# Kernel tuning notes

Hardware: AMD Instinct MI355X
Metric: run time of the kernel (lower is better)

## Reference

```python
import jax, jax.numpy as jnp
import numpy as np

N_QUBITS = 10
DEPTH = 5
DIM = 2 ** N_QUBITS  # 1024
NUM_CLASSES = 2
BATCH = 16384
IN_DIM = 784


def _rot_matrices(w):
    # w: [depth, n_qubits, 3] angles (phi, theta, omega); qml.Rot = RZ(omega) RY(theta) RZ(phi)
    phi, theta, omega = w[..., 0], w[..., 1], w[..., 2]
    c, s = jnp.cos(theta / 2), jnp.sin(theta / 2)
    e = lambda a: jnp.exp(1j * a.astype(jnp.complex64))
    m00 = e(-(phi + omega) / 2) * c
    m01 = -e((phi - omega) / 2) * s
    m10 = e(-(phi - omega) / 2) * s
    m11 = e((phi + omega) / 2) * c
    return jnp.stack([jnp.stack([m00, m01], -1), jnp.stack([m10, m11], -1)], -2)  # [D, n, 2, 2]


def _apply_1q(state, U, w):
    # state: [B] + [2]*n ; apply 2x2 U on qubit axis w
    s = jnp.moveaxis(state, w + 1, -1)
    s = s @ U.T
    return jnp.moveaxis(s, -1, w + 1)


def _apply_cnot(state, c, t):
    s = jnp.moveaxis(state, (c + 1, t + 1), (-2, -1))
    s = jnp.concatenate([s[..., 0:1, :], s[..., 1:2, ::-1]], axis=-2)  # flip target where control=1
    return jnp.moveaxis(s, (-2, -1), (c + 1, t + 1))


def _circuit(x, weights):
    B = x.shape[0]
    # AmplitudeEmbedding: pad_with=0, normalize=True
    amp = jnp.pad(x, ((0, 0), (0, DIM - x.shape[1])))
    amp = amp / jnp.linalg.norm(amp, axis=1, keepdims=True)
    state = amp.astype(jnp.complex64).reshape((B,) + (2,) * N_QUBITS)
    U = _rot_matrices(weights)
    for d in range(DEPTH):
        for i in range(N_QUBITS):  # entangling CNOT ring
            state = _apply_cnot(state, i, (i + 1) % N_QUBITS)
        for i in range(N_QUBITS):  # per-qubit Rot
            state = _apply_1q(state, U[d, i], i)
    probs = (state.real ** 2 + state.imag ** 2).reshape(B, DIM)
    # <Z_i> = P(bit_i = 0) - P(bit_i = 1)
    z = []
    for i in range(N_QUBITS):
        p = probs.reshape(B, 2 ** i, 2, -1)
        z.append(p[:, :, 0, :].sum((1, 2)) - p[:, :, 1, :].sum((1, 2)))
    return jnp.stack(z, axis=1)  # [B, n_qubits]


def setup_inputs() -> dict:
    key = jax.random.key(0)
    k1, k2, k3 = jax.random.split(key, 3)
    x = jax.random.normal(k1, (BATCH, IN_DIM), dtype=jnp.float32)
    weights = jax.random.uniform(k2, (DEPTH, N_QUBITS, 3), dtype=jnp.float32) * (2.0 * np.pi)
    y = jax.random.randint(k3, (BATCH,), 0, NUM_CLASSES)
    return {"x": x, "weights": weights, "y": y}


def reference(x, weights, y):
    logits = _circuit(x, weights)[:, :NUM_CLASSES]
    logp = jax.nn.log_softmax(logits, axis=-1)
    loss = -jnp.take_along_axis(logp, y[:, None], axis=1).mean()
    return loss
```

## Files before the change

### kernel.cpp

```cpp
#include <hip/hip_runtime.h>
#include <type_traits>

#define NQ 10
#define N_DEPTH 5
#define DIM 1024
#define BATCH 16384
#define IN_DIM 784
#define NGATES 50
#define KALLOC 832
#define NT 13
#define NSLOT 768
#define NB 12

typedef float f32x2 __attribute__((ext_vector_type(2)));
typedef float f32x4 __attribute__((ext_vector_type(4)));
typedef unsigned u32x4 __attribute__((ext_vector_type(4)));

struct MaskTab {
  unsigned v[NGATES];
  unsigned p[NGATES];
  unsigned vz0, vz1;
};

constexpr MaskTab make_masks() {
  MaskTab t{};
  unsigned v[NQ], p[NQ];
  for (int i = 0; i < NQ; ++i) { v[i] = 1u << (9 - i); p[i] = 1u << (9 - i); }
  for (int d = 0; d < N_DEPTH; ++d) {
    for (int i = 0; i < NQ; ++i) {
      int c = i, tt = (i + 1) % NQ;
      v[tt] ^= v[c];
      p[c]  ^= p[tt];
    }
    for (int i = 0; i < NQ; ++i) {
      t.v[d * NQ + i] = v[i];
      t.p[d * NQ + i] = p[i];
    }
  }
  t.vz0 = v[0];
  t.vz1 = v[1];
  return t;
}

constexpr MaskTab MT = make_masks();

struct PermTab { short slot[DIM]; };
constexpr PermTab make_perm() {
  PermTab t{};
  int a = 0, b = 256, c = 512;
  for (int m = 0; m < DIM; ++m) {
    const int p0 = __builtin_popcount((unsigned)m & MT.vz0) & 1;
    const int p1 = __builtin_popcount((unsigned)m & MT.vz1) & 1;
    if (p0 && !p1)      t.slot[m] = (short)a++;
    else if (!p0 && p1) t.slot[m] = (short)b++;
    else if (p0 && p1)  t.slot[m] = (short)c++;
    else                t.slot[m] = -1;
  }
  return t;
}
__constant__ PermTab d_PT = make_perm();

struct BitPlan { int wpos[2]; int rpos[2]; int lpos[6]; unsigned wmask; };
constexpr BitPlan make_plan() {
  BitPlan bp{};
  int bestc = 1000; unsigned best = 3;
  for (int a = 0; a < NQ; ++a)
    for (int b = a + 1; b < NQ; ++b) {
      unsigned m = (1u << a) | (1u << b);
      int c = 0;
      for (int g = 0; g < NGATES; ++g) if (MT.p[g] & m) ++c;
      if (c < bestc) { bestc = c; best = m; }
    }
  bp.wmask = best;
  int rem[NQ]; int nr = 0, wi = 0;
  for (int b = 0; b < NQ; ++b) {
    if (best & (1u << b)) bp.wpos[wi++] = b;
    else rem[nr++] = b;
  }
  for (int i = 0; i < 6; ++i) bp.lpos[i] = rem[i];
  bp.rpos[0] = rem[6]; bp.rpos[1] = rem[7];
  return bp;
}
constexpr BitPlan BP = make_plan();

constexpr unsigned gath_l(unsigned p) {
  unsigned r = 0;
  for (int i = 0; i < 6; ++i) if (p & (1u << BP.lpos[i])) r |= 1u << i;
  return r;
}
constexpr unsigned gath_r(unsigned p) {
  unsigned r = 0;
  for (int i = 0; i < 2; ++i) if (p & (1u << BP.rpos[i])) r |= 1u << i;
  return r;
}
constexpr unsigned scat_r(unsigned x) {
  return ((x & 1u) << BP.rpos[0]) | (((x >> 1) & 1u) << BP.rpos[1]);
}
constexpr int ncross_before(int g) {
  int c = 0;
  for (int i = 0; i < g; ++i) if (MT.p[i] & BP.wmask) ++c;
  return c;
}

template <int I, int N, typename F>
__device__ __forceinline__ void static_for(F&& f) {
  if constexpr (I < N) {
    f(std::integral_constant<int, I>{});
    static_for<I + 1, N>(static_cast<F&&>(f));
  }
}

constexpr int xcost(unsigned m) {
  constexpr int t[16] = {0,1,1,1,2,2,2,1,1,2,2,2,2,2,2,1};
  return t[m & 15u] + (((m >> 4) & 1u) ? 3 : 0) + (((m >> 5) & 1u) ? 3 : 0);
}

template <int CTRL>
__device__ __forceinline__ float dppf(float x) {
  int xi = (int)__float_as_uint(x);
  return __uint_as_float(
      (unsigned)__builtin_amdgcn_update_dpp(xi, xi, CTRL, 0xF, 0xF, false));
}

__device__ __forceinline__ float plswap16(float x) {
  float a = x, b = x;
  asm("s_nop 1\n\t"
      "v_permlane16_swap_b32 %0, %1" : "+v"(a), "+v"(b));
  return (a + b) - x;
}
__device__ __forceinline__ float plswap32(float x) {
  float a = x, b = x;
  asm("s_nop 1\n\t"
      "v_permlane32_swap_b32 %0, %1" : "+v"(a), "+v"(b));
  return (a + b) - x;
}

template <unsigned M>
__device__ __forceinline__ float xlane_f(float x) {
  float r = x;
  constexpr unsigned m4 = M & 15u;
  if constexpr (m4 == 1u)  r = dppf<0x0B1>(r);
  else if constexpr (m4 == 2u)  r = dppf<0x04E>(r);
  else if constexpr (m4 == 3u)  r = dppf<0x01B>(r);
  else if constexpr (m4 == 4u)  { r = dppf<0x141>(r); r = dppf<0x01B>(r); }
  else if constexpr (m4 == 5u)  { r = dppf<0x141>(r); r = dppf<0x04E>(r); }
  else if constexpr (m4 == 6u)  { r = dppf<0x141>(r); r = dppf<0x0B1>(r); }
  else if constexpr (m4 == 7u)  r = dppf<0x141>(r);
  else if constexpr (m4 == 8u)  r = dppf<0x128>(r);
  else if constexpr (m4 == 9u)  { r = dppf<0x128>(r); r = dppf<0x0B1>(r); }
  else if constexpr (m4 == 10u) { r = dppf<0x128>(r); r = dppf<0x04E>(r); }
  else if constexpr (m4 == 11u) { r = dppf<0x128>(r); r = dppf<0x01B>(r); }
  else if constexpr (m4 == 12u) { r = dppf<0x140>(r); r = dppf<0x01B>(r); }
  else if constexpr (m4 == 13u) { r = dppf<0x140>(r); r = dppf<0x04E>(r); }
  else if constexpr (m4 == 14u) { r = dppf<0x140>(r); r = dppf<0x0B1>(r); }
  else if constexpr (m4 == 15u) r = dppf<0x140>(r);
  if constexpr ((M & 16u) != 0u) r = plswap16(r);
  if constexpr ((M & 32u) != 0u) r = plswap32(r);
  return r;
}

template <unsigned M>
__device__ __forceinline__ f32x2 xchg(f32x2 v) {
  if constexpr (M == 0u) {
    return v;
  } else if constexpr (xcost(M) >= 5) {
    f32x2 r;
    r.x = __shfl_xor(v.x, (int)M);
    r.y = __shfl_xor(v.y, (int)M);
    return r;
  } else {
    f32x2 r;
    r.x = xlane_f<M>(v.x);
    r.y = xlane_f<M>(v.y);
    return r;
  }
}

__device__ __forceinline__ f32x2 ampfma(f32x2 o, f32x2 q, f32x2 co, f32x2 cp) {
  f32x2 d;
  asm("v_pk_mul_f32 %0, %2, %1 op_sel:[0,0] op_sel_hi:[0,1]\n\t"
      "v_pk_fma_f32 %0, %2, %1, %0 op_sel:[1,1,0] op_sel_hi:[1,0,1] neg_lo:[1,0,0]\n\t"
      "v_pk_fma_f32 %0, %3, %4, %0 op_sel:[0,0,0] op_sel_hi:[0,1,1]\n\t"
      "v_pk_fma_f32 %0, %3, %4, %0 op_sel:[1,1,0] op_sel_hi:[1,0,1] neg_lo:[1,0,0]"
      : "=&v"(d)
      : "v"(o), "v"(co), "v"(cp), "v"(q));
  return d;
}

__device__ __forceinline__ float fxor(float x, unsigned m) {
  return __uint_as_float(__float_as_uint(x) ^ m);
}

__device__ __forceinline__ unsigned pk4_fp8(float a, float b, float c, float d) {
  int v = __builtin_amdgcn_cvt_pk_fp8_f32(a, b, 0, false);
  v = __builtin_amdgcn_cvt_pk_fp8_f32(c, d, v, true);
  return (unsigned)v;
}

__device__ __forceinline__ void gll16(const void* g, void* l) {
  __builtin_amdgcn_global_load_lds(
      (const __attribute__((address_space(1))) void*)g,
      (__attribute__((address_space(3))) void*)l, 16, 0, 0);
}

#define XSCALE 32.0f
#define WSCALE 16.0f
#define SINV   (1.0f / 262144.0f)

__global__ __launch_bounds__(256) void prep(const float* __restrict__ X,
                                            char* __restrict__ Xf8,
                                            float* __restrict__ xn2,
                                            const float* __restrict__ w,
                                            unsigned short* __restrict__ W2u) {
  __shared__ f32x4 UL4[NGATES];
  __shared__ f32x2 S0[DIM];
  __shared__ f32x2 S1[DIM];

  const int tid = threadIdx.x;

  if (blockIdx.x >= 832) {
    const int row = (blockIdx.x - 832) * 8 + (tid >> 5);
    const int l32 = tid & 31;
    const float* src = X + (size_t)row * IN_DIM;
    char* dst = Xf8 + (size_t)row * KALLOC;
    float ssq = 0.0f;
    for (int c = l32; c < 52; c += 32) {
      u32x4 out;
      if (c < 49) {
        f32x4 v0 = *(const f32x4*)(src + c * 16);
        f32x4 v1 = *(const f32x4*)(src + c * 16 + 4);
        f32x4 v2 = *(const f32x4*)(src + c * 16 + 8);
        f32x4 v3 = *(const f32x4*)(src + c * 16 + 12);
        ssq += v0.x * v0.x + v0.y * v0.y + v0.z * v0.z + v0.w * v0.w +
               v1.x * v1.x + v1.y * v1.y + v1.z * v1.z + v1.w * v1.w +
               v2.x * v2.x + v2.y * v2.y + v2.z * v2.z + v2.w * v2.w +
               v3.x * v3.x + v3.y * v3.y + v3.z * v3.z + v3.w * v3.w;
        out = u32x4{
          pk4_fp8(v0.x * XSCALE, v0.y * XSCALE, v0.z * XSCALE, v0.w * XSCALE),
          pk4_fp8(v1.x * XSCALE, v1.y * XSCALE, v1.z * XSCALE, v1.w * XSCALE),
          pk4_fp8(v2.x * XSCALE, v2.y * XSCALE, v2.z * XSCALE, v2.w * XSCALE),
          pk4_fp8(v3.x * XSCALE, v3.y * XSCALE, v3.z * XSCALE, v3.w * XSCALE)};
      } else {
        out = u32x4{0, 0, 0, 0};
      }
      *(u32x4*)(dst + c * 16) = out;
    }
#pragma unroll
    for (int off = 1; off < 32; off <<= 1) ssq += __shfl_xor(ssq, off);
    if (l32 == 0) xn2[row] = ssq;
    return;
  }

  if (tid < NGATES) {
    float phi = w[tid * 3 + 0], th = w[tid * 3 + 1], om = w[tid * 3 + 2];
    float ct = cosf(th * 0.5f), st = sinf(th * 0.5f);
    float aa = (phi + om) * 0.5f, bb = (phi - om) * 0.5f;
    float cA = cosf(aa), sA = sinf(aa), cB = cosf(bb), sB = sinf(bb);
    UL4[tid] = f32x4{ ct * cA, -ct * sA, -st * cB, -st * sB };
  }

  const int j = blockIdx.x;
  unsigned short* rowp = W2u + (size_t)j * NSLOT;

  if (j >= IN_DIM) {
#pragma unroll
    for (int k = 0; k < 3; ++k) rowp[tid + k * 256] = 0;
    return;
  }

  const int wv = tid >> 6, lane = tid & 63;
  unsigned mbase = ((unsigned)(wv & 1) << BP.wpos[0]) |
                   ((unsigned)(wv >> 1) << BP.wpos[1]);
#pragma unroll
  for (int i = 0; i < 6; ++i)
    mbase |= (((unsigned)lane >> i) & 1u) << BP.lpos[i];

  f32x2 a[4];
  static_for<0, 4>([&](auto R_) {
    constexpr int r = decltype(R_)::value;
    constexpr unsigned rs = scat_r((unsigned)r);
    a[r] = f32x2{((mbase | rs) == (unsigned)j) ? 1.0f : 0.0f, 0.0f};
  });
  __syncthreads();

  static_for<0, NGATES>([&](auto G_) {
    constexpr int G = decltype(G_)::value;
    constexpr unsigned p = MT.p[G];
    constexpr unsigned v = MT.v[G];
    constexpr unsigned pw = p & BP.wmask;
    const f32x4 A = UL4[G];

    if constexpr (pw == 0u) {
      constexpr unsigned lx = gath_l(p);
      constexpr unsigned rx = gath_r(p);
      if constexpr (rx == 0u) {
        static_for<0, 4>([&](auto R_) {
          constexpr int r = decltype(R_)::value;
          constexpr unsigned rs = scat_r((unsigned)r);
          f32x2 o = a[r];
          f32x2 q = xchg<lx>(o);
          const unsigned sg =
              (unsigned)(__popc((int)((mbase | rs) & v)) & 1) << 31;
          const f32x2 co = {A.x, fxor(A.y, sg)};
          const f32x2 cp = {fxor(A.z, sg), A.w};
          a[r] = ampfma(o, q, co, cp);
        });
      } else {
        static_for<0, 4>([&](auto R_) {
          constexpr int r = decltype(R_)::value;
          constexpr int r2 = r ^ (int)rx;
          if constexpr (r < r2) {
            constexpr unsigned rs0 = scat_r((unsigned)r);
            constexpr unsigned rs1 = scat_r((unsigned)r2);
            f32x2 o0 = a[r], o1 = a[r2];
            f32x2 q0 = xchg<lx>(o1);
            f32x2 q1 = xchg<lx>(o0);
            const unsigned sg0 =
                (unsigned)(__popc((int)((mbase | rs0) & v)) & 1) << 31;
            const unsigned sg1 =
                (unsigned)(__popc((int)((mbase | rs1) & v)) & 1) << 31;
            const f32x2 co0 = {A.x, fxor(A.y, sg0)};
            const f32x2 cp0 = {fxor(A.z, sg0), A.w};
            const f32x2 co1 = {A.x, fxor(A.y, sg1)};
            const f32x2 cp1 = {fxor(A.z, sg1), A.w};
            a[r]  = ampfma(o0, q0, co0, cp0);
            a[r2] = ampfma(o1, q1, co1, cp1);
          }
        });
      }
    } else {
      constexpr int cidx = ncross_before(G);
      f32x2* S = (cidx & 1) ? S1 : S0;
      static_for<0, 4>([&](auto R_) {
        constexpr int r = decltype(R_)::value;
        constexpr unsigned rs = scat_r((unsigned)r);
        S[mbase | rs] = a[r];
      });
      __syncthreads();
      static_for<0, 4>([&](auto R_) {
        constexpr int r = decltype(R_)::value;
        constexpr unsigned rs = scat_r((unsigned)r);
        const unsigned m = mbase | rs;
        f32x2 o = a[r];
        f32x2 q = S[m ^ p];
        const unsigned sg = (unsigned)(__popc((int)(m & v)) & 1) << 31;
        const f32x2 co = {A.x, fxor(A.y, sg)};
        const f32x2 cp = {fxor(A.z, sg), A.w};
        a[r] = ampfma(o, q, co, cp);
      });
    }
  });

  static_for<0, 4>([&](auto R_) {
    constexpr int r = decltype(R_)::value;
    constexpr unsigned rs = scat_r((unsigned)r);
    const unsigned m = mbase | rs;
    const int s = d_PT.slot[m];
    if (s >= 0)
      rowp[s] = (unsigned short)(pk4_fp8(a[r].x * WSCALE, a[r].y * WSCALE,
                                         0.0f, 0.0f) & 0xffffu);
  });
}

__global__ __launch_bounds__(256) void transpose_w(const unsigned* __restrict__ W2u32,
                                                   unsigned* __restrict__ W2Tu32) {
  __shared__ unsigned tile[64][33];
  const int j0 = blockIdx.x * 64;
  const int s0 = blockIdx.y * 64;
  const int t = threadIdx.x;
#pragma unroll
  for (int i = 0; i < 8; ++i) {
    const int idx = i * 256 + t;
    const int jr = idx >> 5, sc = idx & 31;
    tile[jr][sc] = W2u32[(size_t)(j0 + jr) * (NSLOT / 2) + (s0 >> 1) + sc];
  }
  __syncthreads();
#pragma unroll
  for (int i = 0; i < 8; ++i) {
    const int idx = i * 256 + t;
    const int rl = idx >> 4, jq = idx & 15;
    const int slot = rl >> 1, c = rl & 1;
    const int sc = slot >> 1, p = slot & 1;
    unsigned out = 0;
#pragma unroll
    for (int q = 0; q < 4; ++q) {
      const unsigned w32 = tile[jq * 4 + q][sc];
      const unsigned h = (w32 >> (16 * p)) & 0xffffu;
      out |= ((h >> (8 * c)) & 0xffu) << (8 * q);
    }
    const int orow = 2 * (s0 + slot) + c;
    W2Tu32[((size_t)orow * KALLOC + j0 + jq * 4) >> 2] = out;
  }
}

__global__ __launch_bounds__(512) void gemm_fused(const char* __restrict__ Xf8,
                                                  const char* __restrict__ W2T,
                                                  float* __restrict__ accb) {
  __shared__ u32x4 lds4[3072];
  char* lds = (char*)lds4;

  const int tid = threadIdx.x;
  const int orig = blockIdx.x;
  const int bx = (orig & 7) * 96 + (orig >> 3);
  const int mb = bx / NB, nb = bx % NB;
  const int m0 = mb * 256, n0 = nb * 128;
  const int lane = tid & 63, wv = tid >> 6;
  const int wm = wv >> 2, wn = wv & 3;

  const int rl = lane >> 2;
  const int csrc = (lane & 3) ^ (rl & 3) ^ ((rl >> 2) & 3);

  auto stage = [&](int t) {
    char* Ab = lds + (t & 1) * 24576;
    char* Bb = Ab + 16384;
    const int col = t * 64 + csrc * 16;
#pragma unroll
    for (int i = 0; i < 2; ++i) {
      const int g = wv * 2 + i;
      const int row = g * 16 + rl;
      gll16(Xf8 + (size_t)(m0 + row) * KALLOC + col, Ab + g * 1024);
    }
    {
      const int row = wv * 16 + rl;
      gll16(W2T + (size_t)(n0 + row) * KALLOC + col, Bb + wv * 1024);
    }
  };

  stage(0);
  asm volatile("s_waitcnt vmcnt(0)" ::: "memory");
  __builtin_amdgcn_s_barrier();

  f32x4 acc[8][2];
#pragma unroll
  for (int fm = 0; fm < 8; ++fm)
#pragma unroll
    for (int fn = 0; fn < 2; ++fn) acc[fm][fn] = f32x4{0, 0, 0, 0};

  const int kc = lane >> 4;

  for (int t = 0; t < NT; ++t) {
    const char* Ab = lds + (t & 1) * 24576;
    const char* Bb = Ab + 16384;

    long af0[8], bf0[2], af1[8], bf1[2];
#pragma unroll
    for (int f = 0; f < 8; ++f) {
      const int ar = wm * 128 + f * 16 + (lane & 15);
      const int sw = (ar & 3) ^ ((ar >> 2) & 3);
      af0[f] = *(const long*)(Ab + ar * 64 + (((kc >> 1) ^ sw) * 16) + (kc & 1) * 8);
    }
#pragma unroll
    for (int f = 0; f < 2; ++f) {
      const int br = wn * 32 + f * 16 + (lane & 15);
      const int sw = (br & 3) ^ ((br >> 2) & 3);
      bf0[f] = *(const long*)(Bb + br * 64 + (((kc >> 1) ^ sw) * 16) + (kc & 1) * 8);
    }
    if (t < NT - 1) stage(t + 1);
#pragma unroll
    for (int f = 0; f < 8; ++f) {
      const int ar = wm * 128 + f * 16 + (lane & 15);
      const int sw = (ar & 3) ^ ((ar >> 2) & 3);
      const int kb = 4 + kc;
      af1[f] = *(const long*)(Ab + ar * 64 + (((kb >> 1) ^ sw) * 16) + (kb & 1) * 8);
    }
#pragma unroll
    for (int f = 0; f < 2; ++f) {
      const int br = wn * 32 + f * 16 + (lane & 15);
      const int sw = (br & 3) ^ ((br >> 2) & 3);
      const int kb = 4 + kc;
      bf1[f] = *(const long*)(Bb + br * 64 + (((kb >> 1) ^ sw) * 16) + (kb & 1) * 8);
    }

    __builtin_amdgcn_s_setprio(1);
#pragma unroll
    for (int fm = 0; fm < 8; ++fm)
#pragma unroll
      for (int fn = 0; fn < 2; ++fn)
        acc[fm][fn] = __builtin_amdgcn_mfma_f32_16x16x32_fp8_fp8(
            af0[fm], bf0[fn], acc[fm][fn], 0, 0, 0);
    __builtin_amdgcn_s_setprio(0);

    __builtin_amdgcn_s_setprio(1);
#pragma unroll
    for (int fm = 0; fm < 8; ++fm)
#pragma unroll
      for (int fn = 0; fn < 2; ++fn)
        acc[fm][fn] = __builtin_amdgcn_mfma_f32_16x16x32_fp8_fp8(
            af1[fm], bf1[fn], acc[fm][fn], 0, 0, 0);
    __builtin_amdgcn_s_setprio(0);

    if (t < NT - 1) {
      asm volatile("s_waitcnt vmcnt(0)" ::: "memory");
      __builtin_amdgcn_sched_barrier(0);
      __builtin_amdgcn_s_barrier();
    }
  }

#pragma unroll
  for (int fm = 0; fm < 8; ++fm) {
    float sn[4] = {0, 0, 0, 0};
#pragma unroll
    for (int fn = 0; fn < 2; ++fn) {
#pragma unroll
      for (int r = 0; r < 4; ++r) {
        const float vv = acc[fm][fn][r];
        sn[r] = fmaf(vv, vv, sn[r]);
      }
    }
#pragma unroll
    for (int off = 1; off < 16; off <<= 1) {
#pragma unroll
      for (int r = 0; r < 4; ++r) sn[r] += __shfl_xor(sn[r], off);
    }
    if ((lane & 15) == 0) {
#pragma unroll
      for (int r = 0; r < 4; ++r) {
        const int m = m0 + wm * 128 + fm * 16 + (lane >> 4) * 4 + r;
        accb[(size_t)nb * BATCH + m] = sn[r];
      }
    }
  }
}

__global__ __launch_bounds__(256) void loss_partial(const float* __restrict__ accb,
                                                    const float* __restrict__ xn2,
                                                    const int* __restrict__ y,
                                                    float* __restrict__ partial) {
  const int s = blockIdx.x * 256 + threadIdx.x;
  float SA = 0.0f, SB = 0.0f, SC = 0.0f;
#pragma unroll
  for (int k = 0; k < 4; ++k) {
    SA += accb[(size_t)(0 + k) * BATCH + s];
    SB += accb[(size_t)(4 + k) * BATCH + s];
    SC += accb[(size_t)(8 + k) * BATCH + s];
  }
  SA *= SINV; SB *= SINV; SC *= SINV;
  const float n2 = xn2[s];
  const float z0 = n2 - 2.0f * (SA + SC);
  const float z1 = n2 - 2.0f * (SB + SC);
  const float inv = 1.0f / n2;
  const float l0 = z0 * inv, l1 = z1 * inv;
  const float mx = fmaxf(l0, l1);
  const float lse = mx + logf(expf(l0 - mx) + expf(l1 - mx));
  float loss = lse - ((y[s] == 0) ? l0 : l1);

  __shared__ float sm[256];
  sm[threadIdx.x] = loss;
  __syncthreads();
  for (int st = 128; st > 0; st >>= 1) {
    if (threadIdx.x < st) sm[threadIdx.x] += sm[threadIdx.x + st];
    __syncthreads();
  }
  if (threadIdx.x == 0) partial[blockIdx.x] = sm[0];
}

__global__ __launch_bounds__(64) void loss_final(const float* __restrict__ partial,
                                                 float* __restrict__ out) {
  float v = partial[threadIdx.x];
#pragma unroll
  for (int off = 1; off < 64; off <<= 1) v += __shfl_xor(v, off);
  if (threadIdx.x == 0) out[0] = v * (1.0f / (float)BATCH);
}

extern "C" void kernel_launch(void* const* d_in, const int* in_sizes, int n_in,
                              void* d_out, int out_size, void* d_ws, size_t ws_size,
                              hipStream_t stream) {
  const float* x = (const float*)d_in[0];
  const float* w = (const float*)d_in[1];
  const int*   y = (const int*)d_in[2];

  char* ws = (char*)d_ws;
  char*     Xf8  = ws;
  unsigned short* W2u = (unsigned short*)(ws + 13631488);
  char*     W2Tu = ws + 14909440;
  float*    xn2  = (float*)(ws + 16187392);
  float*    accb = (float*)(ws + 16252928);
  float* partial = (float*)(ws + 17039360);

  prep<<<2880, 256, 0, stream>>>(x, Xf8, xn2, w, W2u);
  transpose_w<<<dim3(13, 12), 256, 0, stream>>>((const unsigned*)W2u,
                                                (unsigned*)W2Tu);
  gemm_fused<<<768, 512, 0, stream>>>(Xf8, W2Tu, accb);
  loss_partial<<<BATCH / 256, 256, 0, stream>>>(accb, xn2, y, partial);
  loss_final<<<1, 64, 0, stream>>>(partial, (float*)d_out);
}
```

Measured before the change: 77.10 us.

## Switch GEMM to scaled 16x16x128 FP8 MFMA with K padded to 896

The fp8 GEMM now uses the MI355X scaled MFMA 16x16x128 instruction with unit scales in place of pairs of 16x16x32 fp8 MFMAs. K is padded from 832 to 896 so it splits into 7 tiles of 128, and transpose_w gains a block that zero-fills the new padding. The LDS tile layout changes to 128-byte rows with an XOR swizzle. The double-buffered prefetch is replaced by a single buffer with load, wait, barrier, compute on each tile, so global loads no longer overlap MFMA work. This trades fewer, wider MFMA issues for lost load/compute overlap and some extra padded K work.

```diff
diff --git a/kernel.cpp b/kernel.cpp
--- a/kernel.cpp
+++ b/kernel.cpp
@@ -7,14 +7,15 @@
 #define BATCH 16384
 #define IN_DIM 784
 #define NGATES 50
-#define KALLOC 832
-#define NT 13
+#define KALLOC 896
+#define NTK 7
 #define NSLOT 768
 #define NB 12
 
 typedef float f32x2 __attribute__((ext_vector_type(2)));
 typedef float f32x4 __attribute__((ext_vector_type(4)));
 typedef unsigned u32x4 __attribute__((ext_vector_type(4)));
+typedef int i32x8 __attribute__((ext_vector_type(8)));
 
 struct MaskTab {
   unsigned v[NGATES];
@@ -206,6 +207,7 @@
 #define XSCALE 32.0f
 #define WSCALE 16.0f
 #define SINV   (1.0f / 262144.0f)
+#define UNIT_SCALE 0x7F7F7F7F
 
 __global__ __launch_bounds__(256) void prep(const float* __restrict__ X,
                                             char* __restrict__ Xf8,
@@ -224,7 +226,7 @@
     const float* src = X + (size_t)row * IN_DIM;
     char* dst = Xf8 + (size_t)row * KALLOC;
     float ssq = 0.0f;
-    for (int c = l32; c < 52; c += 32) {
+    for (int c = l32; c < 56; c += 32) {
       u32x4 out;
       if (c < 49) {
         f32x4 v0 = *(const f32x4*)(src + c * 16);
@@ -368,6 +370,18 @@
   const int j0 = blockIdx.x * 64;
   const int s0 = blockIdx.y * 64;
   const int t = threadIdx.x;
+
+  if (j0 == 832) {
+#pragma unroll
+    for (int i = 0; i < 8; ++i) {
+      const int idx = i * 256 + t;
+      const int rl = idx >> 4, jq = idx & 15;
+      const int orow = 2 * s0 + rl;
+      W2Tu32[((size_t)orow * KALLOC + 832 + jq * 4) >> 2] = 0u;
+    }
+    return;
+  }
+
 #pragma unroll
   for (int i = 0; i < 8; ++i) {
     const int idx = i * 256 + t;
@@ -407,68 +421,63 @@
   const int lane = tid & 63, wv = tid >> 6;
   const int wm = wv >> 2, wn = wv & 3;
 
-  const int rl = lane >> 2;
-  const int csrc = (lane & 3) ^ (rl & 3) ^ ((rl >> 2) & 3);
+  const int rl = lane >> 3;
+  const int csrc = (lane & 7) ^ rl;
+
+  char* Ab = lds;
+  char* Bb = lds + 32768;
 
   auto stage = [&](int t) {
-    char* Ab = lds + (t & 1) * 24576;
-    char* Bb = Ab + 16384;
-    const int col = t * 64 + csrc * 16;
+    const int col = t * 128 + csrc * 16;
+#pragma unroll
+    for (int i = 0; i < 4; ++i) {
+      const int g = wv * 4 + i;
+      const int row = g * 8 + rl;
+      gll16(Xf8 + (size_t)(m0 + row) * KALLOC + col, Ab + g * 1024);
+    }
 #pragma unroll
     for (int i = 0; i < 2; ++i) {
       const int g = wv * 2 + i;
-      const int row = g * 16 + rl;
-      gll16(Xf8 + (size_t)(m0 + row) * KALLOC + col, Ab + g * 1024);
-    }
-    {
-      const int row = wv * 16 + rl;
-      gll16(W2T + (size_t)(n0 + row) * KALLOC + col, Bb + wv * 1024);
+      const int row = g * 8 + rl;
+      gll16(W2T + (size_t)(n0 + row) * KALLOC + col, Bb + g * 1024);
     }
   };
 
-  stage(0);
-  asm volatile("s_waitcnt vmcnt(0)" ::: "memory");
-  __builtin_amdgcn_s_barrier();
-
   f32x4 acc[8][2];
 #pragma unroll
   for (int fm = 0; fm < 8; ++fm)
 #pragma unroll
     for (int fn = 0; fn < 2; ++fn) acc[fm][fn] = f32x4{0, 0, 0, 0};
 
-  const int kc = lane >> 4;
-
-  for (int t = 0; t < NT; ++t) {
-    const char* Ab = lds + (t & 1) * 24576;
-    const char* Bb = Ab + 16384;
-
-    long af0[8], bf0[2], af1[8], bf1[2];
+  const int kq = lane >> 4;
+
+  for (int t = 0; t < NTK; ++t) {
+    stage(t);
+    asm volatile("s_waitcnt vmcnt(0)" ::: "memory");
+    __builtin_amdgcn_s_barrier();
+
+    i32x8 af[8], bf[2];
 #pragma unroll
     for (int f = 0; f < 8; ++f) {
       const int ar = wm * 128 + f * 16 + (lane & 15);
-      const int sw = (ar & 3) ^ ((ar >> 2) & 3);
-      af0[f] = *(const long*)(Ab + ar * 64 + (((kc >> 1) ^ sw) * 16) + (kc & 1) * 8);
+      const char* base = Ab + ar * 128;
+      u32x4 lo = *(const u32x4*)(base + (((2 * kq) ^ (ar & 7)) * 16));
+      u32x4 hi = *(const u32x4*)(base + (((2 * kq + 1) ^ (ar & 7)) * 16));
+      i32x8 v;
+      v[0] = (int)lo.x; v[1] = (int)lo.y; v[2] = (int)lo.z; v[3] = (int)lo.w;
+      v[4] = (int)hi.x; v[5] = (int)hi.y; v[6] = (int)hi.z; v[7] = (int)hi.w;
+      af[f] = v;
     }
 #pragma unroll
     for (int f = 0; f < 2; ++f) {
       const int br = wn * 32 + f * 16 + (lane & 15);
-      const int sw = (br & 3) ^ ((br >> 2) & 3);
-      bf0[f] = *(const long*)(Bb + br * 64 + (((kc >> 1) ^ sw) * 16) + (kc & 1) * 8);
-    }
-    if (t < NT - 1) stage(t + 1);
-#pragma unroll
-    for (int f = 0; f < 8; ++f) {
-      const int ar = wm * 128 + f * 16 + (lane & 15);
-      const int sw = (ar & 3) ^ ((ar >> 2) & 3);
-      const int kb = 4 + kc;
-      af1[f] = *(const long*)(Ab + ar * 64 + (((kb >> 1) ^ sw) * 16) + (kb & 1) * 8);
-    }
-#pragma unroll
-    for (int f = 0; f < 2; ++f) {
-      const int br = wn * 32 + f * 16 + (lane & 15);
-      const int sw = (br & 3) ^ ((br >> 2) & 3);
-      const int kb = 4 + kc;
-      bf1[f] = *(const long*)(Bb + br * 64 + (((kb >> 1) ^ sw) * 16) + (kb & 1) * 8);
+      const char* base = Bb + br * 128;
+      u32x4 lo = *(const u32x4*)(base + (((2 * kq) ^ (br & 7)) * 16));
+      u32x4 hi = *(const u32x4*)(base + (((2 * kq + 1) ^ (br & 7)) * 16));
+      i32x8 v;
+      v[0] = (int)lo.x; v[1] = (int)lo.y; v[2] = (int)lo.z; v[3] = (int)lo.w;
+      v[4] = (int)hi.x; v[5] = (int)hi.y; v[6] = (int)hi.z; v[7] = (int)hi.w;
+      bf[f] = v;
     }
 
     __builtin_amdgcn_s_setprio(1);
@@ -476,24 +485,12 @@
     for (int fm = 0; fm < 8; ++fm)
 #pragma unroll
       for (int fn = 0; fn < 2; ++fn)
-        acc[fm][fn] = __builtin_amdgcn_mfma_f32_16x16x32_fp8_fp8(
-            af0[fm], bf0[fn], acc[fm][fn], 0, 0, 0);
+        acc[fm][fn] = __builtin_amdgcn_mfma_scale_f32_16x16x128_f8f6f4(
+            af[fm], bf[fn], acc[fm][fn], 0, 0,
+            0, UNIT_SCALE, 0, UNIT_SCALE);
     __builtin_amdgcn_s_setprio(0);
 
-    __builtin_amdgcn_s_setprio(1);
-#pragma unroll
-    for (int fm = 0; fm < 8; ++fm)
-#pragma unroll
-      for (int fn = 0; fn < 2; ++fn)
-        acc[fm][fn] = __builtin_amdgcn_mfma_f32_16x16x32_fp8_fp8(
-            af1[fm], bf1[fn], acc[fm][fn], 0, 0, 0);
-    __builtin_amdgcn_s_setprio(0);
-
-    if (t < NT - 1) {
-      asm volatile("s_waitcnt vmcnt(0)" ::: "memory");
-      __builtin_amdgcn_sched_barrier(0);
-      __builtin_amdgcn_s_barrier();
-    }
+    if (t < NTK - 1) __builtin_amdgcn_s_barrier();
   }
 
 #pragma unroll
@@ -571,14 +568,14 @@
 
   char* ws = (char*)d_ws;
   char*     Xf8  = ws;
-  unsigned short* W2u = (unsigned short*)(ws + 13631488);
-  char*     W2Tu = ws + 14909440;
-  float*    xn2  = (float*)(ws + 16187392);
-  float*    accb = (float*)(ws + 16252928);
-  float* partial = (float*)(ws + 17039360);
+  unsigned short* W2u = (unsigned short*)(ws + 14680064);
+  char*     W2Tu = ws + 15958016;
+  float*    xn2  = (float*)(ws + 17334272);
+  float*    accb = (float*)(ws + 17399808);
+  float* partial = (float*)(ws + 18186240);
 
   prep<<<2880, 256, 0, stream>>>(x, Xf8, xn2, w, W2u);
-  transpose_w<<<dim3(13, 12), 256, 0, stream>>>((const unsigned*)W2u,
+  transpose_w<<<dim3(14, 12), 256, 0, stream>>>((const unsigned*)W2u,
                                                 (unsigned*)W2Tu);
   gemm_fused<<<768, 512, 0, stream>>>(Xf8, W2Tu, accb);
   loss_partial<<<BATCH / 256, 256, 0, stream>>>(accb, xn2, y, partial);
```

Result: slower. 118.1 us (+53.2%).
